# Kernel optimization log

Hardware: AMD Instinct MI355X
Metric: run time of the kernel (lower is better)

The kernel has to match this reference:

```python
import jax, jax.numpy as jnp
import numpy as np
import math

T, B = 512, 32
QD, SD, H, NH = 128, 256, 512, 8
NQ, NS, NSUB = 30000, 400, 8
DKEY = QD + 2 * SD      # 640
DVAL = 4 * SD + QD      # 1152
P = H + 2 * SD + QD     # 1152 (pred_in_feature)
DH = H // NH            # 64
NEG = -1e32


def _layernorm(x, g, b, eps=1e-5):
    mu = jnp.mean(x, axis=-1, keepdims=True)
    var = jnp.mean((x - mu) ** 2, axis=-1, keepdims=True)
    return (x - mu) * jax.lax.rsqrt(var + eps) * g + b


def setup_inputs() -> dict:
    key = jax.random.key(0)
    ks = iter(jax.random.split(key, 48))
    def nrm(shape, scale=0.05):
        return (scale * jax.random.normal(next(ks), shape)).astype(jnp.float32)
    inp = {}
    inp['ans'] = jax.random.randint(next(ks), (T, B), 1, 5, dtype=jnp.int32)
    inp['correct_ans'] = jax.random.randint(next(ks), (T, B), 1, 5, dtype=jnp.int32)
    inp['labels'] = jax.random.randint(next(ks), (T, B), 0, 2, dtype=jnp.int32)
    inp['mask'] = jnp.ones((T, B), jnp.float32)
    inp['q_ids'] = jax.random.randint(next(ks), (T, B), 0, NQ, dtype=jnp.int32)
    inp['subject_ids'] = jax.random.randint(next(ks), (T, B, NSUB), 0, NS, dtype=jnp.int32)
    inp['subject_mask'] = (jax.random.uniform(next(ks), (T, B, NSUB)) < 0.7).astype(jnp.float32)
    inp['Eq'] = nrm((NQ, QD)); inp['Es'] = nrm((NS, SD))
    inp['Ea'] = nrm((4, SD)); inp['El'] = nrm((2, SD))
    inp['Wq'] = nrm((H, DKEY)); inp['bq'] = jnp.zeros((H,), jnp.float32)
    inp['Wk'] = nrm((H, DKEY)); inp['bk'] = jnp.zeros((H,), jnp.float32)
    inp['Wv'] = nrm((H, DVAL)); inp['bv'] = jnp.zeros((H,), jnp.float32)
    inp['Wo'] = nrm((H, H)); inp['bo'] = jnp.zeros((H,), jnp.float32)
    inp['ln1_g'] = jnp.ones((H,), jnp.float32); inp['ln1_b'] = jnp.zeros((H,), jnp.float32)
    inp['W1'] = nrm((H, H)); inp['b1'] = jnp.zeros((H,), jnp.float32)
    inp['W2'] = nrm((H, H)); inp['b2'] = jnp.zeros((H,), jnp.float32)
    inp['ln2_g'] = jnp.ones((H,), jnp.float32); inp['ln2_b'] = jnp.zeros((H,), jnp.float32)
    inp['gammas'] = jnp.zeros((NH, 1, 1), jnp.float32)
    inp['L1W'] = nrm((P, P)); inp['L1b'] = jnp.zeros((P,), jnp.float32)
    inp['L2W'] = nrm((P, P)); inp['L2b'] = jnp.zeros((P,), jnp.float32)
    inp['OW'] = nrm((1, P)); inp['Ob'] = jnp.zeros((1,), jnp.float32)
    return inp


def _forward(ans, correct_ans, labels, q_ids, subject_ids,
             mask, subject_mask, Eq, Es, Ea, El,
             Wq, bq, Wk, bk, Wv, bv, Wo, bo, ln1_g, ln1_b,
             W1, b1, W2, b2, ln2_g, ln2_b, gammas,
             L1W, L1b, L2W, L2b, OW, Ob):
    m3 = mask[:, :, None]                                   # [T,B,1]
    subjects = jnp.sum(Es[subject_ids] * subject_mask[..., None], axis=2)   # [T,B,SD]
    questions = Eq[q_ids]                                   # [T,B,QD]
    ans_embed = Ea[ans - 1] * m3
    ca_embed = Ea[correct_ans - 1]
    lab_embed = El[labels] * m3
    query = jnp.concatenate([questions, subjects, ca_embed], axis=-1)       # [T,B,DKEY]
    value = jnp.concatenate([lab_embed, ans_embed, ca_embed, questions, subjects], axis=-1)  # [T,B,DVAL]
    # note: original applies q_linear to kk and k_linear to qq (qq==kk==query here); akt=True => no pos-embed
    q = (query @ Wq.T + bq).reshape(T, B, NH, DH).transpose(1, 2, 0, 3)     # [B,NH,T,DH]
    k = (query @ Wk.T + bk).reshape(T, B, NH, DH).transpose(1, 2, 0, 3)
    v = (value @ Wv.T + bv).reshape(T, B, NH, DH).transpose(1, 2, 0, 3)
    scores = jnp.einsum('bhqd,bhkd->bhqk', q, k) / math.sqrt(DH)            # [B,NH,T,T]
    scores = jnp.where(mask.T[:, None, None, :] == 0, NEG, scores)
    # exponential distance decay (Softplus-gamma), applied AFTER the key-pad fill as in the original
    idx = jnp.arange(T)
    pe = jnp.sqrt(jnp.abs(idx[None, :] - idx[:, None]).astype(jnp.float32)) # [T,T]
    total_effect = jnp.clip(jnp.exp(pe[None] * (-jax.nn.softplus(gammas))), 1e-5, 1e5)  # [NH,T,T]
    scores = scores * total_effect[None]
    causal_bad = jnp.triu(jnp.ones((T, T), bool))            # upper incl. diagonal is masked
    scores = jnp.where(causal_bad, NEG, scores)
    scores = jax.nn.softmax(scores, axis=-1)
    scores = scores.at[:, :, 0, :].set(0.0)                  # pad-zero first query row
    attn = jnp.einsum('bhqk,bhkd->bhqd', scores, v)
    concat = attn.transpose(2, 0, 1, 3).reshape(T, B, H)
    out = _layernorm(concat @ Wo.T + bo, ln1_g, ln1_b)
    ffn = jax.nn.relu(out @ W1.T + b1) @ W2.T + b2
    out = out + _layernorm(ffn, ln2_g, ln2_b)
    pred = jnp.concatenate([out, questions, subjects, ca_embed], axis=-1)   # [T,B,P]
    h = jax.nn.relu(pred @ L1W.T + L1b)
    h = jax.nn.relu(h @ L2W.T + L2b)
    logits = ((h + pred) @ OW.T + Ob)[..., 0]                # [T,B]
    y = labels.astype(jnp.float32)
    bce = jnp.maximum(logits, 0.0) - logits * y + jnp.log1p(jnp.exp(-jnp.abs(logits)))
    loss = jnp.mean(bce * mask) / jnp.mean(mask)
    return loss


def reference(ans, correct_ans, labels, mask, q_ids, subject_ids, subject_mask,
              Eq, Es, Ea, El, Wq, bq, Wk, bk, Wv, bv, Wo, bo, ln1_g, ln1_b,
              W1, b1, W2, b2, ln2_g, ln2_b, gammas, L1W, L1b, L2W, L2b, OW, Ob):
    return _forward(ans, correct_ans, labels, q_ids, subject_ids,
                    mask, subject_mask, Eq, Es, Ea, El,
                    Wq, bq, Wk, bk, Wv, bv, Wo, bo, ln1_g, ln1_b,
                    W1, b1, W2, b2, ln2_g, ln2_b, gammas,
                    L1W, L1b, L2W, L2b, OW, Ob)
```

## Files before the change

kernel.cpp:

```cpp
#include <hip/hip_runtime.h>
#include <math.h>

#define T_LEN 512
#define B_SZ  32
#define NHEAD 8
#define DHEAD 64
#define H_DIM 512
#define TBTOK 16384
#define P_DIM 1152
#define P_PAD 1280

typedef unsigned short ushort_t;
typedef short short8 __attribute__((ext_vector_type(8)));
typedef float f32x4 __attribute__((ext_vector_type(4)));

__device__ __forceinline__ ushort_t f2bf(float f) {
    union { float f; unsigned int u; } v; v.f = f;
    unsigned int r = v.u + 0x7fffu + ((v.u >> 16) & 1u);
    return (ushort_t)(r >> 16);
}
__device__ __forceinline__ float bf2f(ushort_t h) {
    union { unsigned int u; float f; } v; v.u = ((unsigned int)h) << 16;
    return v.f;
}
__device__ __forceinline__ void gload_lds16(const void* g, void* l) {
    __builtin_amdgcn_global_load_lds(
        (const __attribute__((address_space(1))) void*)g,
        (__attribute__((address_space(3))) void*)l, 16, 0, 0);
}

__global__ __launch_bounds__(256) void convert_weights(
    const float* __restrict__ wq, const float* __restrict__ wk,
    const float* __restrict__ wv, const float* __restrict__ wo,
    const float* __restrict__ w1, const float* __restrict__ w2,
    ushort_t* __restrict__ dst, float* __restrict__ accum)
{
    if (blockIdx.x == 0 && threadIdx.x < 2) accum[threadIdx.x] = 0.f;
    const unsigned int offs[7] = {0u, 327680u, 655360u, 1245184u, 1507328u,
                                  1769472u, 2031616u};
    unsigned int c = (blockIdx.x * 256 + threadIdx.x) * 4;
    const float* srcs[6] = {wq, wk, wv, wo, w1, w2};
    int s = 0;
#pragma unroll
    for (int i = 0; i < 5; i++) s += (c >= offs[i + 1]) ? 1 : 0;
    float4 v = *(const float4*)(srcs[s] + (c - offs[s]));
    ushort4 o;
    o.x = f2bf(v.x); o.y = f2bf(v.y); o.z = f2bf(v.z); o.w = f2bf(v.w);
    *(ushort4*)(dst + c) = o;
}

__global__ __launch_bounds__(256) void pad_weights(
    const float* __restrict__ l1, const float* __restrict__ l2,
    const float* __restrict__ L1b, const float* __restrict__ L2b,
    const float* __restrict__ OW,
    ushort_t* __restrict__ l1d, ushort_t* __restrict__ l2d,
    float* __restrict__ L1bp, float* __restrict__ L2bp, float* __restrict__ OWp)
{
    int blk = blockIdx.x;
    if (blk < 1440) {
        int o4 = (blk * 256 + threadIdx.x) * 4;
        int row = o4 / 1152;
        int col = o4 - row * 1152;
        ushort4 o; o.x = 0; o.y = 0; o.z = 0; o.w = 0;
        if (row < 1152) {
            float4 v = *(const float4*)(l1 + (size_t)row * 1152 + col);
            o.x = f2bf(v.x); o.y = f2bf(v.y); o.z = f2bf(v.z); o.w = f2bf(v.w);
        }
        *(ushort4*)(l1d + o4) = o;
    } else if (blk < 3040) {
        int o4 = ((blk - 1440) * 256 + threadIdx.x) * 4;
        int row = o4 / 1280;
        int col = o4 - row * 1280;
        ushort4 o; o.x = 0; o.y = 0; o.z = 0; o.w = 0;
        if (row < 1152 && col < 1152) {
            float4 v = *(const float4*)(l2 + (size_t)row * 1152 + col);
            o.x = f2bf(v.x); o.y = f2bf(v.y); o.z = f2bf(v.z); o.w = f2bf(v.w);
        }
        *(ushort4*)(l2d + o4) = o;
    } else {
        for (int i = threadIdx.x; i < P_PAD; i += 256) {
            L1bp[i] = (i < P_DIM) ? L1b[i] : 0.f;
            L2bp[i] = (i < P_DIM) ? L2b[i] : 0.f;
            OWp[i]  = (i < P_DIM) ? OW[i]  : 0.f;
        }
    }
}

__global__ __launch_bounds__(256) void embed_kernel(
    const int* __restrict__ ans, const int* __restrict__ cans,
    const int* __restrict__ labels, const float* __restrict__ mask,
    const int* __restrict__ qids, const int* __restrict__ sids,
    const float* __restrict__ smask,
    const float* __restrict__ Eq, const float* __restrict__ Es,
    const float* __restrict__ Ea, const float* __restrict__ El,
    ushort_t* __restrict__ pred_bf, ushort_t* __restrict__ value_bf,
    const float* __restrict__ OW, const float* __restrict__ Ob,
    float* __restrict__ lgits)
{
    __shared__ float red[4];
    int m = blockIdx.x;
    int tid = threadIdx.x;
    float mval = mask[m];
    int qid = qids[m];
    int a   = ans[m] - 1;
    int ca  = cans[m] - 1;
    int lb  = labels[m];
    ushort_t* pr = pred_bf  + (size_t)m * P_DIM;
    ushort_t* vr = value_bf + (size_t)m * P_DIM;

    float part = 0.f;
    if (tid < 128) {
        ushort_t qv = f2bf(Eq[(size_t)qid * 128 + tid]);
        pr[512 + tid] = qv;
        vr[768 + tid] = qv;
        part = bf2f(qv) * OW[512 + tid];
    }
    int d = tid;
    float s = 0.f;
#pragma unroll
    for (int j = 0; j < 8; j++) {
        int  sid = sids[m * 8 + j];
        float sm = smask[m * 8 + j];
        s += Es[(size_t)sid * 256 + d] * sm;
    }
    ushort_t sb = f2bf(s);
    pr[640 + d] = sb;
    vr[896 + d] = sb;
    ushort_t cab = f2bf(Ea[ca * 256 + d]);
    pr[896 + d] = cab;
    vr[512 + d] = cab;
    vr[256 + d] = f2bf(Ea[a * 256 + d] * mval);
    vr[0   + d] = f2bf(El[lb * 256 + d] * mval);

    part = fmaf(bf2f(sb),  OW[640 + d], part);
    part = fmaf(bf2f(cab), OW[896 + d], part);
#pragma unroll
    for (int off = 32; off >= 1; off >>= 1) part += __shfl_xor(part, off, 64);
    if ((tid & 63) == 0) red[tid >> 6] = part;
    __syncthreads();
    if (tid == 0) lgits[m] = red[0] + red[1] + red[2] + red[3] + Ob[0];
}

template<int JC, int MODE, bool RELU>
__global__ __launch_bounds__(512, 2) void gemm4p(
    const ushort_t* __restrict__ A, int lda,
    const ushort_t* __restrict__ W, int ldw,
    const float* __restrict__ bias, const float* __restrict__ bias2,
    ushort_t* __restrict__ Cb, ushort_t* __restrict__ Cb2, int ldc, int K,
    const float* __restrict__ OW, float* __restrict__ lg)
{
    constexpr int BN = JC * 64;
    __shared__ __align__(16) ushort_t As2[2][2][256 * 32];
    __shared__ __align__(16) ushort_t Bs2[2][2][BN * 32];

    const int m0 = blockIdx.x * 256;
    const int n0 = blockIdx.y * BN;
    const int tid  = threadIdx.x;
    const int wave = tid >> 6;
    const int lane = tid & 63;
    const int wm = wave >> 2, wn = wave & 3;
    const int fr   = lane & 15;
    const int quad = lane >> 4;
    const int csw  = ((quad + ((fr >> 1) & 3)) & 3) * 8;

    const int slr = lane >> 2;
    const int sc  = (((lane & 3) - ((lane >> 3) & 3)) & 3) * 8;
    const ushort_t* Asrc;
    size_t aRS;
    if (MODE == 4) {
        Asrc = A + ((size_t)(((m0 & 511) + slr) << 5) + (m0 >> 9)) * lda + sc;
        aRS  = (size_t)32 * lda;
    } else {
        Asrc = A + (size_t)(m0 + slr) * lda + sc;
        aRS  = (size_t)lda;
    }
    const ushort_t* Wsrc = W + (size_t)(n0 + slr) * ldw + sc;
    const int NT = K >> 6;

    auto stA = [&](int t, int kh) {
#pragma unroll
        for (int n = 0; n < 2; n++) {
            int rl = (wave + 8 * n) << 4;
            gload_lds16(Asrc + (size_t)rl * aRS + (t * 64 + kh * 32),
                        &As2[t & 1][kh][rl * 32]);
        }
    };
    auto stB = [&](int t, int kh) {
#pragma unroll
        for (int n = 0; n < JC / 2; n++) {
            int rl = (wave + 8 * n) << 4;
            gload_lds16(Wsrc + (size_t)rl * ldw + (t * 64 + kh * 32),
                        &Bs2[t & 1][kh][rl * 32]);
        }
        if (JC & 1) {
            if (wave < 4) {
                int rl = (wave + 8 * (JC / 2)) << 4;
                gload_lds16(Wsrc + (size_t)rl * ldw + (t * 64 + kh * 32),
                            &Bs2[t & 1][kh][rl * 32]);
            }
        }
    };
    auto waitSteady = [&]() {
        if (JC == 2)      asm volatile("s_waitcnt vmcnt(3)" ::: "memory");
        else if (JC == 4) asm volatile("s_waitcnt vmcnt(4)" ::: "memory");
        else {
            if (wave < 4) asm volatile("s_waitcnt vmcnt(5)" ::: "memory");
            else          asm volatile("s_waitcnt vmcnt(4)" ::: "memory");
        }
    };

    f32x4 acc[8][JC] = {};

    stA(0, 0); stB(0, 0); stA(0, 1); stB(0, 1);
    if (NT > 1) { stA(1, 0); stB(1, 0); }
    if (NT > 2) waitSteady();
    else        asm volatile("s_waitcnt vmcnt(0)" ::: "memory");
    __builtin_amdgcn_s_barrier();

    short8 af[4], bf[JC];
    for (int t = 0; t < NT; ++t) {
        const int db = t & 1;
        const ushort_t* Ar0 = &As2[db][0][0];
        const ushort_t* Ar1 = &As2[db][1][0];
        const ushort_t* Br0 = &Bs2[db][0][0];
        const ushort_t* Br1 = &Bs2[db][1][0];

#pragma unroll
        for (int i = 0; i < 4; i++)
            af[i] = *(const short8*)&Ar0[(wm * 128 + i * 16 + fr) * 32 + csw];
#pragma unroll
        for (int j = 0; j < JC; j++)
            bf[j] = *(const short8*)&Br0[(wn * (JC * 16) + j * 16 + fr) * 32 + csw];
        if (t + 1 < NT) stA(t + 1, 1);
        __builtin_amdgcn_s_barrier();
        __builtin_amdgcn_s_setprio(1);
#pragma unroll
        for (int i = 0; i < 4; i++)
#pragma unroll
            for (int j = 0; j < JC; j++)
                acc[i][j] = __builtin_amdgcn_mfma_f32_16x16x32_bf16(
                    af[i], bf[j], acc[i][j], 0, 0, 0);
        __builtin_amdgcn_s_setprio(0);
        __builtin_amdgcn_s_barrier();

#pragma unroll
        for (int i = 0; i < 4; i++)
            af[i] = *(const short8*)&Ar0[(wm * 128 + 64 + i * 16 + fr) * 32 + csw];
        if (t + 1 < NT) stB(t + 1, 1);
        __builtin_amdgcn_s_barrier();
        __builtin_amdgcn_s_setprio(1);
#pragma unroll
        for (int i = 0; i < 4; i++)
#pragma unroll
            for (int j = 0; j < JC; j++)
                acc[4 + i][j] = __builtin_amdgcn_mfma_f32_16x16x32_bf16(
                    af[i], bf[j], acc[4 + i][j], 0, 0, 0);
        __builtin_amdgcn_s_setprio(0);
        __builtin_amdgcn_s_barrier();

#pragma unroll
        for (int i = 0; i < 4; i++)
            af[i] = *(const short8*)&Ar1[(wm * 128 + i * 16 + fr) * 32 + csw];
#pragma unroll
        for (int j = 0; j < JC; j++)
            bf[j] = *(const short8*)&Br1[(wn * (JC * 16) + j * 16 + fr) * 32 + csw];
        if (t + 2 < NT) stA(t + 2, 0);
        __builtin_amdgcn_s_barrier();
        __builtin_amdgcn_s_setprio(1);
#pragma unroll
        for (int i = 0; i < 4; i++)
#pragma unroll
            for (int j = 0; j < JC; j++)
                acc[i][j] = __builtin_amdgcn_mfma_f32_16x16x32_bf16(
                    af[i], bf[j], acc[i][j], 0, 0, 0);
        __builtin_amdgcn_s_setprio(0);
        __builtin_amdgcn_s_barrier();

#pragma unroll
        for (int i = 0; i < 4; i++)
            af[i] = *(const short8*)&Ar1[(wm * 128 + 64 + i * 16 + fr) * 32 + csw];
        if (t + 2 < NT) stB(t + 2, 0);
        if (t + 2 < NT) waitSteady();
        else            asm volatile("s_waitcnt vmcnt(0)" ::: "memory");
        __builtin_amdgcn_s_barrier();
        __builtin_amdgcn_s_setprio(1);
#pragma unroll
        for (int i = 0; i < 4; i++)
#pragma unroll
            for (int j = 0; j < JC; j++)
                acc[4 + i][j] = __builtin_amdgcn_mfma_f32_16x16x32_bf16(
                    af[i], bf[j], acc[4 + i][j], 0, 0, 0);
        __builtin_amdgcn_s_setprio(0);
        __builtin_amdgcn_s_barrier();
    }

    const int nbase = n0 + wn * (JC * 16);

    if (MODE == 3) {
#pragma unroll
        for (int ii = 0; ii < 8; ii++)
#pragma unroll
            for (int r = 0; r < 4; r++) {
                int row = m0 + wm * 128 + (ii >> 2) * 64 + (ii & 3) * 16 + quad * 4 + r;
                float part = 0.f;
#pragma unroll
                for (int j = 0; j < JC; j++) {
                    int col = nbase + j * 16 + fr;
                    float v = fmaxf(acc[ii][j][r] + bias[col], 0.f);
                    part = fmaf(v, OW[col], part);
                }
                part += __shfl_xor(part, 1, 64);
                part += __shfl_xor(part, 2, 64);
                part += __shfl_xor(part, 4, 64);
                part += __shfl_xor(part, 8, 64);
                if (fr == 0) atomicAdd(&lg[row], part);
            }
        return;
    }

    if (MODE == 5) {
        bool side = (nbase >= 512);
        const float* bp = side ? bias2 : bias;
        const int boff  = nbase & 511;
        const float scl = side ? 1.f : 0.125f;
        ushort_t* base  = side ? Cb2 : Cb;
        const int h = (nbase >> 6) & 7;
        ushort_t* etw = ((ushort_t*)As2) + wave * (16 * 72);
#pragma unroll
        for (int ii = 0; ii < 8; ii++) {
#pragma unroll
            for (int r = 0; r < 4; r++)
#pragma unroll
                for (int j = 0; j < 4; j++) {
                    float v = (acc[ii][j][r] + bp[boff + j * 16 + fr]) * scl;
                    etw[(quad * 4 + r) * 72 + j * 16 + fr] = f2bf(v);
                }
            int rowb = m0 + wm * 128 + (ii >> 2) * 64 + (ii & 3) * 16;
#pragma unroll
            for (int u = lane; u < 128; u += 64) {
                int rr = u >> 3, cc = (u & 7) * 8;
                int row = rowb + rr;
                int tq = row >> 5, b = row & 31;
                short8 val = *(const short8*)&etw[rr * 72 + cc];
                *(short8*)&base[(((size_t)(b * 8 + h)) << 15) + ((size_t)tq << 6) + cc] = val;
            }
        }
        return;
    }

    if (MODE == 4) {
        ushort_t* etw = ((ushort_t*)As2) + wave * (32 * 72);
        const int h = nbase >> 6;
        const int dbase = nbase & 63;
#pragma unroll
        for (int mh = 0; mh < 2; mh++) {
#pragma unroll
            for (int i = 0; i < 4; i++)
#pragma unroll
                for (int r = 0; r < 4; r++) {
                    int rl = i * 16 + quad * 4 + r;
#pragma unroll
                    for (int j = 0; j < 2; j++) {
                        int cl = j * 16 + fr;
                        float v = acc[mh * 4 + i][j][r] + bias[nbase + cl];
                        etw[cl * 72 + rl] = f2bf(v);
                    }
                }
            int mbase = m0 + wm * 128 + mh * 64;
            int b = mbase >> 9, t0 = mbase & 511;
            size_t obase = (((size_t)(b * 8 + h)) << 15) + ((size_t)dbase << 9) + t0;
#pragma unroll
            for (int u = lane; u < 256; u += 64) {
                int dr = u >> 3, cc = (u & 7) * 8;
                short8 val = *(const short8*)&etw[dr * 72 + cc];
                *(short8*)&Cb[obase + ((size_t)dr << 9) + cc] = val;
            }
        }
        return;
    }

    {
        constexpr int STR = JC * 16 + 8;
        constexpr int CPR = 2 * JC;
        ushort_t* etw = ((ushort_t*)As2) + wave * (16 * STR);
#pragma unroll
        for (int ii = 0; ii < 8; ii++) {
#pragma unroll
            for (int r = 0; r < 4; r++)
#pragma unroll
                for (int j = 0; j < JC; j++) {
                    float v = acc[ii][j][r] + bias[nbase + j * 16 + fr];
                    if (RELU) v = fmaxf(v, 0.f);
                    etw[(quad * 4 + r) * STR + j * 16 + fr] = f2bf(v);
                }
            int rowb = m0 + wm * 128 + (ii >> 2) * 64 + (ii & 3) * 16;
#pragma unroll
            for (int u = lane; u < 16 * CPR; u += 64) {
                int rr = u / CPR;
                int cc = u - rr * CPR;
                short8 val = *(const short8*)&etw[rr * STR + cc * 8];
                *(short8*)&Cb[(size_t)(rowb + rr) * ldc + nbase + cc * 8] = val;
            }
        }
    }
}

__global__ __launch_bounds__(256) void attn_mfma(
    const ushort_t* __restrict__ qb, const ushort_t* __restrict__ kb,
    const ushort_t* __restrict__ vtb, const float* __restrict__ mask,
    const float* __restrict__ gammas, ushort_t* __restrict__ attnc)
{
    __shared__ __align__(16) ushort_t kbuf[2][64 * 64];
    __shared__ __align__(16) ushort_t vbuf[2][64 * 64];
    __shared__ __align__(16) ushort_t ps[4][16][72];
    __shared__ float decayF[512];
    __shared__ float mneg[512];

    const int bh  = blockIdx.x;
    const int b   = bh >> 3;
    const int h   = bh & 7;
    const int qt0 = (7 - blockIdx.y) * 64;
    const int tid  = threadIdx.x;
    const int wave = tid >> 6;
    const int lane = tid & 63;
    const int fr   = lane & 15;
    const int quad = lane >> 4;

    {
        float g  = gammas[h];
        float sp = (g > 20.f) ? g : log1pf(expf(g));
        for (int i = tid; i < 512; i += 256) {
            decayF[i] = fmaxf(exp2f(-sp * 1.44269504f * sqrtf((float)i)), 1e-5f)
                        * 1.44269504f;
            mneg[i]   = (mask[(size_t)i * B_SZ + b] == 0.f) ? -1e32f : 0.f;
        }
    }

    const int qr0 = qt0 + wave * 16;
    const ushort_t* qbase = qb  + ((size_t)bh << 15);
    const ushort_t* kbase = kb  + ((size_t)bh << 15);
    const ushort_t* vbase = vtb + ((size_t)bh << 15);

    short8 af0 = *(const short8*)(qbase + (size_t)(qr0 + fr) * 64 + quad * 8);
    short8 af1 = *(const short8*)(qbase + (size_t)(qr0 + fr) * 64 + 32 + quad * 8);
    const short8 ones = {0x3F80, 0x3F80, 0x3F80, 0x3F80,
                         0x3F80, 0x3F80, 0x3F80, 0x3F80};

    const int rl0 = wave * 16 + (lane >> 3);
    const int rl1 = rl0 + 8;
    const int sc0 = (((lane & 7) - rl0) & 7) * 8;
    const int sc1 = (((lane & 7) - rl1) & 7) * 8;

    auto stage = [&](int kt, int bufi) {
        gload_lds16(kbase + (size_t)(kt + rl0) * 64 + sc0, &kbuf[bufi][(wave * 16) * 64]);
        gload_lds16(kbase + (size_t)(kt + rl1) * 64 + sc1, &kbuf[bufi][(wave * 16 + 8) * 64]);
        gload_lds16(vbase + (size_t)rl0 * T_LEN + kt + sc0, &vbuf[bufi][(wave * 16) * 64]);
        gload_lds16(vbase + (size_t)rl1 * T_LEN + kt + sc1, &vbuf[bufi][(wave * 16 + 8) * 64]);
    };
    auto frag = [&](const ushort_t* buf, int row, int lchunk) -> short8 {
        return *(const short8*)&buf[row * 64 + ((lchunk + row) & 7) * 8];
    };

    stage(0, 0);

    f32x4 o[4] = {};
    f32x4 lacc = {};
    int bufi = 0;

    for (int kt0 = 0; kt0 <= qt0; kt0 += 64) {
        __syncthreads();
        if (kt0 < qt0) stage(kt0 + 64, bufi ^ 1);
        const bool diag = (kt0 == qt0);
        const ushort_t* kb_ = kbuf[bufi];
        const ushort_t* vb_ = vbuf[bufi];

        f32x4 sacc[4] = {};
#pragma unroll
        for (int j = 0; j < 4; j++) {
            int row = j * 16 + fr;
            short8 k0 = frag(kb_, row, quad);
            short8 k1 = frag(kb_, row, quad + 4);
            sacc[j] = __builtin_amdgcn_mfma_f32_16x16x32_bf16(af0, k0, sacc[j], 0, 0, 0);
            sacc[j] = __builtin_amdgcn_mfma_f32_16x16x32_bf16(af1, k1, sacc[j], 0, 0, 0);
        }

#pragma unroll
        for (int j = 0; j < 4; j++) {
            int kg = kt0 + j * 16 + fr;
            float mn = mneg[kg];
            int qgb = qr0 + quad * 4;
            if (!diag) {
                int base = qgb - kg;
#pragma unroll
                for (int r = 0; r < 4; r++) {
                    float t = fmaf(sacc[j][r], decayF[base + r], mn);
                    union { float f; unsigned u; } cv; cv.f = exp2f(t);
                    ps[wave][quad * 4 + r][j * 16 + fr] = (ushort_t)(cv.u >> 16);
                }
            } else {
#pragma unroll
                for (int r = 0; r < 4; r++) {
                    int didx = qgb + r - kg;
                    float dec = decayF[didx > 0 ? didx : 0];
                    float t = fmaf(sacc[j][r], dec, mn);
                    if (didx <= 0) t = -1e32f;
                    union { float f; unsigned u; } cv; cv.f = exp2f(t);
                    ps[wave][quad * 4 + r][j * 16 + fr] = (ushort_t)(cv.u >> 16);
                }
            }
        }
        short8 pf0 = *(const short8*)&ps[wave][fr][quad * 8];
        short8 pf1 = *(const short8*)&ps[wave][fr][32 + quad * 8];
        lacc = __builtin_amdgcn_mfma_f32_16x16x32_bf16(pf0, ones, lacc, 0, 0, 0);
        lacc = __builtin_amdgcn_mfma_f32_16x16x32_bf16(pf1, ones, lacc, 0, 0, 0);
#pragma unroll
        for (int j2 = 0; j2 < 4; j2++) {
            int row = j2 * 16 + fr;
            short8 v0 = frag(vb_, row, quad);
            short8 v1 = frag(vb_, row, quad + 4);
            o[j2] = __builtin_amdgcn_mfma_f32_16x16x32_bf16(pf0, v0, o[j2], 0, 0, 0);
            o[j2] = __builtin_amdgcn_mfma_f32_16x16x32_bf16(pf1, v1, o[j2], 0, 0, 0);
        }
        bufi ^= 1;
    }

#pragma unroll
    for (int r = 0; r < 4; r++) {
        int qg = qr0 + quad * 4 + r;
        float linv = (qg == 0) ? 0.f : 1.f / lacc[r];
#pragma unroll
        for (int j2 = 0; j2 < 4; j2++)
            ps[wave][quad * 4 + r][j2 * 16 + fr] = f2bf(o[j2][r] * linv);
    }
    const int sub8 = (lane & 7) * 8;
    const int grp  = lane >> 3;
#pragma unroll
    for (int half = 0; half < 2; half++) {
        int rowl = half * 8 + grp;
        short8 val = *(const short8*)&ps[wave][rowl][sub8];
        int qg = qr0 + rowl;
        *(short8*)&attnc[((size_t)qg * B_SZ + b) * H_DIM + h * DHEAD + sub8] = val;
    }
}

__global__ __launch_bounds__(256) void ln1_kernel(
    const ushort_t* __restrict__ X, const float* __restrict__ g,
    const float* __restrict__ bta, ushort_t* __restrict__ Yb)
{
    int m    = blockIdx.x * 4 + (threadIdx.x >> 6);
    int lane = threadIdx.x & 63;
    int c0   = lane * 8;
    const ushort_t* xr = X + (size_t)m * H_DIM + c0;
    float x[8];
    float s = 0.f, ss = 0.f;
    short8 xv = *(const short8*)xr;
#pragma unroll
    for (int i = 0; i < 8; i++) {
        x[i] = bf2f((ushort_t)xv[i]);
        s += x[i]; ss += x[i] * x[i];
    }
#pragma unroll
    for (int off = 32; off >= 1; off >>= 1) {
        s  += __shfl_xor(s,  off, 64);
        ss += __shfl_xor(ss, off, 64);
    }
    float mu  = s * (1.f / 512.f);
    float var = ss * (1.f / 512.f) - mu * mu;
    float rs  = rsqrtf(var + 1e-5f);
    ushort_t yb[8];
#pragma unroll
    for (int i = 0; i < 8; i++)
        yb[i] = f2bf((x[i] - mu) * rs * g[c0 + i] + bta[c0 + i]);
    *(short8*)(Yb + (size_t)m * H_DIM + c0) = *(short8*)&yb[0];
}

__global__ __launch_bounds__(256) void ln2_kernel(
    const ushort_t* __restrict__ X, const float* __restrict__ g,
    const float* __restrict__ bta, const ushort_t* __restrict__ res,
    ushort_t* __restrict__ pred_bf, const float* __restrict__ OW,
    float* __restrict__ lg)
{
    int m    = blockIdx.x * 4 + (threadIdx.x >> 6);
    int lane = threadIdx.x & 63;
    int c0   = lane * 8;
    const ushort_t* xr = X + (size_t)m * H_DIM + c0;
    float x[8];
    float s = 0.f, ss = 0.f;
    short8 xv = *(const short8*)xr;
#pragma unroll
    for (int i = 0; i < 8; i++) {
        x[i] = bf2f((ushort_t)xv[i]);
        s += x[i]; ss += x[i] * x[i];
    }
#pragma unroll
    for (int off = 32; off >= 1; off >>= 1) {
        s  += __shfl_xor(s,  off, 64);
        ss += __shfl_xor(ss, off, 64);
    }
    float mu  = s * (1.f / 512.f);
    float var = ss * (1.f / 512.f) - mu * mu;
    float rs  = rsqrtf(var + 1e-5f);
    short8 rv = *(const short8*)(res + (size_t)m * H_DIM + c0);
    ushort_t yb[8];
    float part = 0.f;
#pragma unroll
    for (int i = 0; i < 8; i++) {
        float v = (x[i] - mu) * rs * g[c0 + i] + bta[c0 + i] + bf2f((ushort_t)rv[i]);
        yb[i] = f2bf(v);
        part = fmaf(v, OW[c0 + i], part);
    }
    *(short8*)(pred_bf + (size_t)m * P_DIM + c0) = *(short8*)&yb[0];
#pragma unroll
    for (int off = 32; off >= 1; off >>= 1) part += __shfl_xor(part, off, 64);
    if (lane == 0) lg[m] += part;
}

__global__ __launch_bounds__(256) void bce_kernel(
    const float* __restrict__ lg, const int* __restrict__ labels,
    const float* __restrict__ mask, float* __restrict__ accum)
{
    int m    = blockIdx.x * 256 + threadIdx.x;
    int lane = threadIdx.x & 63;
    float l  = lg[m];
    float y  = (float)labels[m];
    float mv = mask[m];
    float a  = (fmaxf(l, 0.f) - l * y + log1pf(expf(-fabsf(l)))) * mv;
#pragma unroll
    for (int off = 32; off >= 1; off >>= 1) {
        a  += __shfl_xor(a,  off, 64);
        mv += __shfl_xor(mv, off, 64);
    }
    if (lane == 0) {
        atomicAdd(accum,     a);
        atomicAdd(accum + 1, mv);
    }
}

__global__ void finalize_kernel(const float* __restrict__ accum, float* __restrict__ out)
{
    out[0] = accum[0] / accum[1];
}

extern "C" void kernel_launch(void* const* d_in, const int* in_sizes, int n_in,
                              void* d_out, int out_size, void* d_ws, size_t ws_size,
                              hipStream_t stream)
{
    (void)in_sizes; (void)n_in; (void)out_size;
    const int*   ans    = (const int*)  d_in[0];
    const int*   cans   = (const int*)  d_in[1];
    const int*   labels = (const int*)  d_in[2];
    const float* mask   = (const float*)d_in[3];
    const int*   qids   = (const int*)  d_in[4];
    const int*   sids   = (const int*)  d_in[5];
    const float* smask  = (const float*)d_in[6];
    const float* Eq     = (const float*)d_in[7];
    const float* Es     = (const float*)d_in[8];
    const float* Ea     = (const float*)d_in[9];
    const float* El     = (const float*)d_in[10];
    const float* Wq     = (const float*)d_in[11];
    const float* bq     = (const float*)d_in[12];
    const float* Wk     = (const float*)d_in[13];
    const float* bk     = (const float*)d_in[14];
    const float* Wv     = (const float*)d_in[15];
    const float* bv     = (const float*)d_in[16];
    const float* Wo     = (const float*)d_in[17];
    const float* bo     = (const float*)d_in[18];
    const float* ln1_g  = (const float*)d_in[19];
    const float* ln1_b  = (const float*)d_in[20];
    const float* W1     = (const float*)d_in[21];
    const float* b1     = (const float*)d_in[22];
    const float* W2     = (const float*)d_in[23];
    const float* b2     = (const float*)d_in[24];
    const float* ln2_g  = (const float*)d_in[25];
    const float* ln2_b  = (const float*)d_in[26];
    const float* gammas = (const float*)d_in[27];
    const float* L1W    = (const float*)d_in[28];
    const float* L1b    = (const float*)d_in[29];
    const float* L2W    = (const float*)d_in[30];
    const float* L2b    = (const float*)d_in[31];
    const float* OW     = (const float*)d_in[32];
    const float* Ob     = (const float*)d_in[33];
    float* out = (float*)d_out;

    const size_t U = (size_t)TBTOK * 64;
    if (ws_size < 42 * U * sizeof(float)) return;
    float* ws = (float*)d_ws;
    ushort_t* wtb      = (ushort_t*)(ws);
    ushort_t* pred_bf  = (ushort_t*)(ws + 3 * U);
    ushort_t* value_bf = (ushort_t*)(ws + 12 * U);
    ushort_t* qb       = (ushort_t*)(ws + 21 * U);
    ushort_t* kb       = (ushort_t*)(ws + 25 * U);
    ushort_t* vtb      = (ushort_t*)(ws + 29 * U);
    ushort_t* attnc_bf = (ushort_t*)(ws + 33 * U);
    ushort_t* x1_bf    = (ushort_t*)(ws + 12 * U);
    ushort_t* out1_bf  = (ushort_t*)(ws + 24 * U);
    ushort_t* f1_bf    = (ushort_t*)(ws + 28 * U);
    ushort_t* f2_bf    = (ushort_t*)(ws + 32 * U);
    ushort_t* h1_bf    = (ushort_t*)(ws + 12 * U);
    float*    lgits    = ws + 41 * U;
    float*    accum    = lgits + TBTOK;
    float*    OWp      = accum + 2;
    float*    L1bp     = OWp + P_PAD;
    float*    L2bp     = L1bp + P_PAD;

    ushort_t* wqk_b = wtb + 0;
    ushort_t* wv_b  = wtb + 655360;
    ushort_t* wo_b  = wtb + 1245184;
    ushort_t* w1_b  = wtb + 1507328;
    ushort_t* w2_b  = wtb + 1769472;
    ushort_t* l1_b  = wtb + 2031616;
    ushort_t* l2_b  = wtb + 3506176;

    convert_weights<<<1984, 256, 0, stream>>>(Wq, Wk, Wv, Wo, W1, W2, wtb, accum);
    pad_weights<<<3041, 256, 0, stream>>>(L1W, L2W, L1b, L2b, OW,
                                          l1_b, l2_b, L1bp, L2bp, OWp);
    embed_kernel<<<TBTOK, 256, 0, stream>>>(ans, cans, labels, mask, qids, sids,
                                            smask, Eq, Es, Ea, El, pred_bf, value_bf,
                                            OW, Ob, lgits);
    gemm4p<4,5,false><<<dim3(64, 4), 512, 0, stream>>>(
        pred_bf + 512, P_DIM, wqk_b, 640, bq, bk, qb, kb, 0, 640, nullptr, nullptr);
    gemm4p<2,4,false><<<dim3(64, 4), 512, 0, stream>>>(
        value_bf, P_DIM, wv_b, P_DIM, bv, nullptr, vtb, nullptr, 0, P_DIM, nullptr, nullptr);
    attn_mfma<<<dim3(B_SZ * NHEAD, 8), 256, 0, stream>>>(
        qb, kb, vtb, mask, gammas, attnc_bf);
    gemm4p<2,1,false><<<dim3(64, 4), 512, 0, stream>>>(
        attnc_bf, H_DIM, wo_b, H_DIM, bo, nullptr, x1_bf, nullptr, H_DIM, H_DIM, nullptr, nullptr);
    ln1_kernel<<<TBTOK/4, 256, 0, stream>>>(x1_bf, ln1_g, ln1_b, out1_bf);
    gemm4p<2,1,true><<<dim3(64, 4), 512, 0, stream>>>(
        out1_bf, H_DIM, w1_b, H_DIM, b1, nullptr, f1_bf, nullptr, H_DIM, H_DIM, nullptr, nullptr);
    gemm4p<2,1,false><<<dim3(64, 4), 512, 0, stream>>>(
        f1_bf, H_DIM, w2_b, H_DIM, b2, nullptr, f2_bf, nullptr, H_DIM, H_DIM, nullptr, nullptr);
    ln2_kernel<<<TBTOK/4, 256, 0, stream>>>(f2_bf, ln2_g, ln2_b, out1_bf, pred_bf, OW, lgits);
    gemm4p<5,1,true><<<dim3(64, 4), 512, 0, stream>>>(
        pred_bf, P_DIM, l1_b, P_DIM, L1bp, nullptr, h1_bf, nullptr, P_PAD, P_DIM, nullptr, nullptr);
    gemm4p<5,3,true><<<dim3(64, 4), 512, 0, stream>>>(
        h1_bf, P_PAD, l2_b, P_PAD, L2bp, nullptr, nullptr, nullptr, 0, P_PAD, OWp, lgits);
    bce_kernel<<<TBTOK/256, 256, 0, stream>>>(lgits, labels, mask, accum);
    finalize_kernel<<<1, 1, 0, stream>>>(accum, out);
}
```

Measured before the change: 425.3 us.

## Double-buffer GEMM register fragments to overlap LDS reads with MFMA

Restructures the GEMM main loop so that A/B fragments for the next MFMA cluster are read from LDS into a second register set while the current cluster computes, instead of reading and then waiting at a barrier before computing. Sched barriers keep the MFMA clusters in order, and the next tile's first fragments are prefetched after the wait/barrier. This aims to hide LDS read latency behind MFMA work at the cost of extra VGPRs for the doubled fragments, which may reduce occupancy or cause spills.

After: 488.0 us. 1.15x slower.

```diff
diff --git a/kernel.cpp b/kernel.cpp
--- a/kernel.cpp
+++ b/kernel.cpp
@@ -208,91 +208,75 @@
             else          asm volatile("s_waitcnt vmcnt(4)" ::: "memory");
         }
     };
+    auto rdA = [&](short8* dst, const ushort_t* base, int mh) {
+#pragma unroll
+        for (int i = 0; i < 4; i++)
+            dst[i] = *(const short8*)
+                &base[(wm * 128 + mh * 64 + i * 16 + fr) * 32 + csw];
+    };
+    auto rdB = [&](short8* dst, const ushort_t* base) {
+#pragma unroll
+        for (int j = 0; j < JC; j++)
+            dst[j] = *(const short8*)
+                &base[(wn * (JC * 16) + j * 16 + fr) * 32 + csw];
+    };
+
+#define MMCL(AH, AF, BF)                                                     \
+    __builtin_amdgcn_sched_barrier(0);                                       \
+    __builtin_amdgcn_s_setprio(1);                                           \
+    _Pragma("unroll")                                                        \
+    for (int i = 0; i < 4; i++)                                              \
+    _Pragma("unroll")                                                        \
+        for (int j = 0; j < JC; j++)                                         \
+            acc[(AH) * 4 + i][j] = __builtin_amdgcn_mfma_f32_16x16x32_bf16(  \
+                (AF)[i], (BF)[j], acc[(AH) * 4 + i][j], 0, 0, 0);            \
+    __builtin_amdgcn_s_setprio(0);
 
     f32x4 acc[8][JC] = {};
+    short8 afA[4], afB[4], bfA[JC], bfB[JC];
 
     stA(0, 0); stB(0, 0); stA(0, 1); stB(0, 1);
     if (NT > 1) { stA(1, 0); stB(1, 0); }
     if (NT > 2) waitSteady();
     else        asm volatile("s_waitcnt vmcnt(0)" ::: "memory");
     __builtin_amdgcn_s_barrier();
-
-    short8 af[4], bf[JC];
+    rdA(afA, &As2[0][0][0], 0);
+    rdB(bfA, &Bs2[0][0][0]);
+
     for (int t = 0; t < NT; ++t) {
         const int db = t & 1;
         const ushort_t* Ar0 = &As2[db][0][0];
         const ushort_t* Ar1 = &As2[db][1][0];
-        const ushort_t* Br0 = &Bs2[db][0][0];
         const ushort_t* Br1 = &Bs2[db][1][0];
 
-#pragma unroll
-        for (int i = 0; i < 4; i++)
-            af[i] = *(const short8*)&Ar0[(wm * 128 + i * 16 + fr) * 32 + csw];
-#pragma unroll
-        for (int j = 0; j < JC; j++)
-            bf[j] = *(const short8*)&Br0[(wn * (JC * 16) + j * 16 + fr) * 32 + csw];
         if (t + 1 < NT) stA(t + 1, 1);
+        rdA(afB, Ar0, 1);
+        MMCL(0, afA, bfA)
         __builtin_amdgcn_s_barrier();
-        __builtin_amdgcn_s_setprio(1);
-#pragma unroll
-        for (int i = 0; i < 4; i++)
-#pragma unroll
-            for (int j = 0; j < JC; j++)
-                acc[i][j] = __builtin_amdgcn_mfma_f32_16x16x32_bf16(
-                    af[i], bf[j], acc[i][j], 0, 0, 0);
-        __builtin_amdgcn_s_setprio(0);
+
+        if (t + 1 < NT) stB(t + 1, 1);
+        rdA(afA, Ar1, 0);
+        rdB(bfB, Br1);
+        MMCL(1, afB, bfA)
         __builtin_amdgcn_s_barrier();
 
-#pragma unroll
-        for (int i = 0; i < 4; i++)
-            af[i] = *(const short8*)&Ar0[(wm * 128 + 64 + i * 16 + fr) * 32 + csw];
-        if (t + 1 < NT) stB(t + 1, 1);
+        if (t + 2 < NT) stA(t + 2, 0);
+        rdA(afB, Ar1, 1);
+        MMCL(0, afA, bfB)
         __builtin_amdgcn_s_barrier();
-        __builtin_amdgcn_s_setprio(1);
-#pragma unroll
-        for (int i = 0; i < 4; i++)
-#pragma unroll
-            for (int j = 0; j < JC; j++)
-                acc[4 + i][j] = __builtin_amdgcn_mfma_f32_16x16x32_bf16(
-                    af[i], bf[j], acc[4 + i][j], 0, 0, 0);
-        __builtin_amdgcn_s_setprio(0);
-        __builtin_amdgcn_s_barrier();
-
-#pragma unroll
-        for (int i = 0; i < 4; i++)
-            af[i] = *(const short8*)&Ar1[(wm * 128 + i * 16 + fr) * 32 + csw];
-#pragma unroll
-        for (int j = 0; j < JC; j++)
-            bf[j] = *(const short8*)&Br1[(wn * (JC * 16) + j * 16 + fr) * 32 + csw];
-        if (t + 2 < NT) stA(t + 2, 0);
-        __builtin_amdgcn_s_barrier();
-        __builtin_amdgcn_s_setprio(1);
-#pragma unroll
-        for (int i = 0; i < 4; i++)
-#pragma unroll
-            for (int j = 0; j < JC; j++)
-                acc[i][j] = __builtin_amdgcn_mfma_f32_16x16x32_bf16(
-                    af[i], bf[j], acc[i][j], 0, 0, 0);
-        __builtin_amdgcn_s_setprio(0);
-        __builtin_amdgcn_s_barrier();
-
-#pragma unroll
-        for (int i = 0; i < 4; i++)
-            af[i] = *(const short8*)&Ar1[(wm * 128 + 64 + i * 16 + fr) * 32 + csw];
+
         if (t + 2 < NT) stB(t + 2, 0);
         if (t + 2 < NT) waitSteady();
         else            asm volatile("s_waitcnt vmcnt(0)" ::: "memory");
         __builtin_amdgcn_s_barrier();
-        __builtin_amdgcn_s_setprio(1);
-#pragma unroll
-        for (int i = 0; i < 4; i++)
-#pragma unroll
-            for (int j = 0; j < JC; j++)
-                acc[4 + i][j] = __builtin_amdgcn_mfma_f32_16x16x32_bf16(
-                    af[i], bf[j], acc[4 + i][j], 0, 0, 0);
-        __builtin_amdgcn_s_setprio(0);
+        if (t + 1 < NT) {
+            rdA(afA, &As2[db ^ 1][0][0], 0);
+            rdB(bfA, &Bs2[db ^ 1][0][0]);
+        }
+        MMCL(1, afB, bfB)
         __builtin_amdgcn_s_barrier();
     }
+#undef MMCL
 
     const int nbase = n0 + wn * (JC * 16);
 
```
